# Kernel tuning notes

Hardware: AMD Instinct MI355X
Metric: run time of the kernel (lower is better)

## Reference

```python
import jax, jax.numpy as jnp
import numpy as np

C_IN = 512
C = 64        # per-head dim
N_HEAD = 8
B, S = 2, 2048


def setup_inputs() -> dict:
    key = jax.random.key(0)
    ks = jax.random.split(key, 9)
    scale = 1.0 / np.sqrt(C_IN)
    return {
        "x": jax.random.normal(ks[0], (B, S, C_IN), dtype=jnp.float32),
        "bias": jax.random.normal(ks[1], (B, N_HEAD, S, S), dtype=jnp.float32),
        "Wq": jax.random.normal(ks[2], (N_HEAD * C, C_IN), dtype=jnp.float32) * scale,
        "Wk": jax.random.normal(ks[3], (N_HEAD * C, C_IN), dtype=jnp.float32) * scale,
        "Wv": jax.random.normal(ks[4], (N_HEAD * C, C_IN), dtype=jnp.float32) * scale,
        "Wo": jax.random.normal(ks[5], (C_IN, N_HEAD * C), dtype=jnp.float32) * scale,
        "bo": jax.random.normal(ks[6], (C_IN,), dtype=jnp.float32) * 0.01,
        "Wg": jax.random.normal(ks[7], (N_HEAD * C, C_IN), dtype=jnp.float32) * scale,
        "bg": jax.random.normal(ks[8], (N_HEAD * C,), dtype=jnp.float32) * 0.01,
    }


def reference(x, bias, Wq, Wk, Wv, Wo, bo, Wg, bg):
    # x: [B, S, C_IN]; attn_dim=1 -> q/k/v axis is already at -2 after movedim.
    # Project and split heads: [B, S, H*C] -> [B, H, S, C]
    def split_heads(t):
        Bq, Sq, _ = t.shape
        return t.reshape(Bq, Sq, N_HEAD, C).transpose(0, 2, 1, 3)

    q = split_heads(x @ Wq.T) / jnp.sqrt(jnp.asarray(C, x.dtype))
    k = split_heads(x @ Wk.T)
    v = split_heads(x @ Wv.T)

    a = jnp.einsum("bhqc,bhkc->bhqk", q, k) + bias   # [B, H, S, S]
    a = jax.nn.softmax(a, axis=-1)
    o = jnp.einsum("bhqk,bhkc->bhqc", a, v)          # [B, H, S, C]

    # merge heads back: [B, S, H*C]
    o = o.transpose(0, 2, 1, 3).reshape(x.shape[0], x.shape[1], N_HEAD * C)
    g = jax.nn.sigmoid(x @ Wg.T + bg)
    o = g * o
    return o @ Wo.T + bo                              # [B, S, C_IN]
```

## Files before the change

kernel.cpp:

```cpp
#include <hip/hip_runtime.h>
#include <math.h>

#define BB 2
#define HH 8
#define SS 2048
#define CC 64
#define CIN 512
#define DDIM 512
#define MM (BB*SS)
#define KCHUNK 32
#define NCHUNK (SS / KCHUNK)
#define NBUF 4

#define LOG2E 1.4426950408889634f
#define SHIFT2 (16.0f * LOG2E)

using short8  = __attribute__((ext_vector_type(8))) short;
using float4v = __attribute__((ext_vector_type(4))) float;

__device__ __forceinline__ unsigned short tob(float f) {
    unsigned u = __float_as_uint(f);
    unsigned r = (u + 0x7fffu + ((u >> 16) & 1u)) >> 16;
    return (unsigned short)r;
}
__device__ __forceinline__ float fromb(unsigned short u) {
    return __uint_as_float(((unsigned)u) << 16);
}

#define GLDS(srcp, ldsp)                                                     \
    __builtin_amdgcn_global_load_lds(                                        \
        (const __attribute__((address_space(1))) void*)(srcp),               \
        (__attribute__((address_space(3))) void*)(ldsp), 16, 0, 0)

__global__ __launch_bounds__(256) void convert_all(
    const float* __restrict__ x,
    const float* __restrict__ wq, const float* __restrict__ wk,
    const float* __restrict__ wv, const float* __restrict__ wg,
    const float* __restrict__ wo,
    unsigned short* __restrict__ xb,
    unsigned short* __restrict__ wqb, unsigned short* __restrict__ wkb,
    unsigned short* __restrict__ wvb, unsigned short* __restrict__ wgb,
    unsigned short* __restrict__ wob)
{
    const int NX4 = MM * CIN / 4;
    int i = blockIdx.x * blockDim.x + threadIdx.x;
    const float* src; unsigned short* dst; float scale = 1.0f; int off;
    if (i < NX4) { src = x; dst = xb; off = i; }
    else {
        int j = i - NX4;
        int seg = j >> 16;
        off = j & 65535;
        if      (seg == 0) { src = wq; dst = wqb; scale = 0.125f * LOG2E; }
        else if (seg == 1) { src = wk; dst = wkb; }
        else if (seg == 2) { src = wv; dst = wvb; }
        else if (seg == 3) { src = wg; dst = wgb; }
        else               { src = wo; dst = wob; }
    }
    float4 v = ((const float4*)src)[off];
    ushort4 o;
    o.x = tob(v.x * scale); o.y = tob(v.y * scale);
    o.z = tob(v.z * scale); o.w = tob(v.w * scale);
    ((ushort4*)dst)[off] = o;
}

__global__ __launch_bounds__(256) void proj_gemm(
    const unsigned short* __restrict__ X,
    const unsigned short* __restrict__ Wq,
    const unsigned short* __restrict__ Wk,
    const unsigned short* __restrict__ Wv,
    const unsigned short* __restrict__ Wg,
    const float* __restrict__ bg,
    unsigned short* __restrict__ Qd,
    unsigned short* __restrict__ Kd,
    unsigned short* __restrict__ Vd,
    unsigned short* __restrict__ Gd)
{
    __shared__ __align__(16) unsigned short At[64][72];
    __shared__ __align__(16) unsigned short Bt[64][72];

    int mode = blockIdx.z;
    const unsigned short* W = (mode == 0) ? Wq : (mode == 1) ? Wk : (mode == 2) ? Wv : Wg;

    int m0 = blockIdx.y * 64;
    int n0 = blockIdx.x * 64;
    int tid = threadIdx.x;
    int w = tid >> 6, lane = tid & 63;
    int quad = lane >> 4, l16 = lane & 15;
    int wm = w & 1, wn = w >> 1;

    float4v acc[2][2];
    for (int a = 0; a < 2; ++a) for (int c = 0; c < 2; ++c) acc[a][c] = (float4v)0.0f;

    for (int kc = 0; kc < CIN; kc += 64) {
        for (int it = 0; it < 2; ++it) {
            int idx = it * 2048 + tid * 8;
            int row = idx >> 6, col = idx & 63;
            *(short8*)&At[row][col] = *(const short8*)&X[(size_t)(m0 + row) * CIN + kc + col];
            *(short8*)&Bt[row][col] = *(const short8*)&W[(size_t)(n0 + row) * CIN + kc + col];
        }
        __syncthreads();
        for (int ks = 0; ks < 2; ++ks) {
            short8 a0 = *(const short8*)&At[wm * 32 + l16][ks * 32 + quad * 8];
            short8 a1 = *(const short8*)&At[wm * 32 + 16 + l16][ks * 32 + quad * 8];
            short8 b0 = *(const short8*)&Bt[wn * 32 + l16][ks * 32 + quad * 8];
            short8 b1 = *(const short8*)&Bt[wn * 32 + 16 + l16][ks * 32 + quad * 8];
            acc[0][0] = __builtin_amdgcn_mfma_f32_16x16x32_bf16(a0, b0, acc[0][0], 0, 0, 0);
            acc[0][1] = __builtin_amdgcn_mfma_f32_16x16x32_bf16(a0, b1, acc[0][1], 0, 0, 0);
            acc[1][0] = __builtin_amdgcn_mfma_f32_16x16x32_bf16(a1, b0, acc[1][0], 0, 0, 0);
            acc[1][1] = __builtin_amdgcn_mfma_f32_16x16x32_bf16(a1, b1, acc[1][1], 0, 0, 0);
        }
        __syncthreads();
    }

    if (mode == 2) {
        for (int a = 0; a < 2; ++a) for (int c = 0; c < 2; ++c)
            for (int r = 0; r < 4; ++r) {
                int ml = wm * 32 + a * 16 + quad * 4 + r;
                int nl = wn * 32 + c * 16 + l16;
                At[nl][ml] = tob(acc[a][c][r]);
            }
        __syncthreads();
        int bi = m0 >> 11, h = n0 >> 6, s0 = m0 & 2047;
        int crow = tid >> 2, seg = tid & 3;
        unsigned short* dp = Vd + (((size_t)(bi * HH + h) * CC) + crow) * SS + s0 + seg * 16;
        *(short8*)dp       = *(const short8*)&At[crow][seg * 16];
        *(short8*)(dp + 8) = *(const short8*)&At[crow][seg * 16 + 8];
        return;
    }

    for (int a = 0; a < 2; ++a) for (int c = 0; c < 2; ++c)
        for (int r = 0; r < 4; ++r) {
            int gm = m0 + wm * 32 + a * 16 + quad * 4 + r;
            int gn = n0 + wn * 32 + c * 16 + l16;
            float v = acc[a][c][r];
            if (mode <= 1) {
                int bi = gm >> 11, s = gm & 2047, h = gn >> 6, cc = gn & 63;
                unsigned short* d = (mode == 0) ? Qd : Kd;
                d[(((size_t)(bi * HH + h) * SS) + s) * CC + cc] = tob(v);
            } else {
                float g = 1.0f / (1.0f + __expf(-(v + bg[gn])));
                Gd[(size_t)gm * DDIM + gn] = tob(g);
            }
        }
}

__global__ __launch_bounds__(256, 2) void attn_kernel(
    const unsigned short* __restrict__ Q,
    const unsigned short* __restrict__ K,
    const unsigned short* __restrict__ V,
    const float* __restrict__ bias,
    const unsigned short* __restrict__ G,
    unsigned short* __restrict__ Om)
{
    __shared__ __align__(16) unsigned short Kt[NBUF][32][64];
    __shared__ __align__(16) unsigned short Vt[NBUF][64][32];
    __shared__ __align__(16) float Bs[NBUF][64][32];
    __shared__ __align__(16) unsigned short Pt[4][16][40];

    int qb = blockIdx.x * 64;
    int bh = blockIdx.y;
    int b = bh >> 3, h = bh & 7;
    int tid = threadIdx.x;
    int w = tid >> 6, lane = tid & 63;
    int quad = lane >> 4, l16 = lane & 15;
    int swl = l16 & 7;
    int vsw = l16 & 3;

    int phase = (blockIdx.x + blockIdx.y) & (NCHUNK - 1);

    const unsigned short* Qbh = Q + (size_t)bh * SS * CC;
    const unsigned short* Kbh = K + (size_t)bh * SS * CC;
    const unsigned short* Vbh = V + (size_t)bh * CC * SS;
    const float* Bbh = bias + (size_t)bh * SS * SS;

    int qrow = qb + w * 16 + l16;
    short8 aq0 = *(const short8*)&Qbh[(size_t)qrow * CC + quad * 8];
    short8 aq1 = *(const short8*)&Qbh[(size_t)qrow * CC + 32 + quad * 8];

    float lsum[4] = {0.f, 0.f, 0.f, 0.f};
    float4v accO[4];
    for (int jn = 0; jn < 4; ++jn) accO[jn] = (float4v)0.0f;

    int row8 = lane >> 3;
    int kswz = (lane & 7) ^ row8;
    int row4 = lane >> 2;
    int vswz = (lane & 3) ^ (row4 & 3);

    auto STAGE = [&](int d, int kb) {
        GLDS(Kbh + (size_t)(kb + w * 8 + row8) * CC + kswz * 8, &Kt[d][w * 8][0]);
        GLDS(Vbh + (size_t)(w * 16 + row4) * SS + kb + vswz * 8, &Vt[d][w * 16][0]);
#pragma unroll
        for (int t = 0; t < 2; ++t)
            GLDS(Bbh + (size_t)(qb + w * 16 + t * 8 + row8) * SS + kb + (lane & 7) * 4,
                 &Bs[d][w * 16 + t * 8][0]);
    };

    STAGE(0, ((0 + phase) & (NCHUNK - 1)) * KCHUNK);
    STAGE(1, ((1 + phase) & (NCHUNK - 1)) * KCHUNK);
    STAGE(2, ((2 + phase) & (NCHUNK - 1)) * KCHUNK);

#pragma unroll 4
    for (int c = 0; c < NCHUNK; ++c) {
        int d = c & (NBUF - 1);
        __builtin_amdgcn_sched_barrier(0);
        if (c + 2 < NCHUNK) {
            asm volatile("s_waitcnt vmcnt(8)" ::: "memory");
        } else if (c + 1 < NCHUNK) {
            asm volatile("s_waitcnt vmcnt(4)" ::: "memory");
        } else {
            asm volatile("s_waitcnt vmcnt(0)" ::: "memory");
        }
        __builtin_amdgcn_sched_barrier(0);
        __builtin_amdgcn_s_barrier();
        __builtin_amdgcn_sched_barrier(0);

        if (c + 3 < NCHUNK)
            STAGE((c + 3) & (NBUF - 1), ((c + 3 + phase) & (NCHUNK - 1)) * KCHUNK);

        float4v sa[2];
#pragma unroll
        for (int j = 0; j < 2; ++j) sa[j] = (float4v)(-SHIFT2);
#pragma unroll
        for (int j = 0; j < 2; ++j) {
            short8 bk0 = *(const short8*)&Kt[d][j * 16 + l16][((quad    ) ^ swl) * 8];
            short8 bk1 = *(const short8*)&Kt[d][j * 16 + l16][((quad + 4) ^ swl) * 8];
            sa[j] = __builtin_amdgcn_mfma_f32_16x16x32_bf16(aq0, bk0, sa[j], 0, 0, 0);
            sa[j] = __builtin_amdgcn_mfma_f32_16x16x32_bf16(aq1, bk1, sa[j], 0, 0, 0);
        }

#pragma unroll
        for (int j = 0; j < 2; ++j)
#pragma unroll
            for (int r = 0; r < 4; ++r) {
                float bb = Bs[d][w * 16 + quad * 4 + r][j * 16 + l16];
                float p = __builtin_amdgcn_exp2f(fmaf(bb, LOG2E, sa[j][r]));
                lsum[r] += p;
                Pt[w][quad * 4 + r][j * 16 + l16] = tob(p);
            }

        {
            short8 ap = *(const short8*)&Pt[w][l16][quad * 8];
#pragma unroll
            for (int jn = 0; jn < 4; ++jn) {
                short8 bv = *(const short8*)&Vt[d][jn * 16 + l16][(quad ^ vsw) * 8];
                accO[jn] = __builtin_amdgcn_mfma_f32_16x16x32_bf16(ap, bv, accO[jn], 0, 0, 0);
            }
        }

        __builtin_amdgcn_sched_barrier(0);
        asm volatile("s_waitcnt lgkmcnt(0)" ::: "memory");
        __builtin_amdgcn_sched_barrier(0);
    }

    float rl[4];
#pragma unroll
    for (int r = 0; r < 4; ++r) {
        float s = lsum[r];
        s += __shfl_xor(s, 1, 64);
        s += __shfl_xor(s, 2, 64);
        s += __shfl_xor(s, 4, 64);
        s += __shfl_xor(s, 8, 64);
        rl[r] = 1.0f / s;
    }

    int mrow = b * SS + qb + w * 16 + quad * 4;
#pragma unroll
    for (int jn = 0; jn < 4; ++jn)
#pragma unroll
        for (int r = 0; r < 4; ++r) {
            int col = h * 64 + jn * 16 + l16;
            float g = fromb(G[(size_t)(mrow + r) * DDIM + col]);
            Om[(size_t)(mrow + r) * DDIM + col] = tob(accO[jn][r] * rl[r] * g);
        }
}

__global__ __launch_bounds__(256) void out_gemm(
    const unsigned short* __restrict__ Og,
    const unsigned short* __restrict__ W,
    const float* __restrict__ bo,
    float* __restrict__ out)
{
    __shared__ __align__(16) unsigned short At[64][72];
    __shared__ __align__(16) unsigned short Bt[64][72];

    int m0 = blockIdx.y * 64;
    int n0 = blockIdx.x * 64;
    int tid = threadIdx.x;
    int w = tid >> 6, lane = tid & 63;
    int quad = lane >> 4, l16 = lane & 15;
    int wm = w & 1, wn = w >> 1;

    float4v acc[2][2];
    for (int a = 0; a < 2; ++a) for (int c = 0; c < 2; ++c) acc[a][c] = (float4v)0.0f;

    for (int kc = 0; kc < DDIM; kc += 64) {
        for (int it = 0; it < 2; ++it) {
            int idx = it * 2048 + tid * 8;
            int row = idx >> 6, col = idx & 63;
            *(short8*)&At[row][col] = *(const short8*)&Og[(size_t)(m0 + row) * DDIM + kc + col];
            *(short8*)&Bt[row][col] = *(const short8*)&W[(size_t)(n0 + row) * DDIM + kc + col];
        }
        __syncthreads();
        for (int ks = 0; ks < 2; ++ks) {
            short8 a0 = *(const short8*)&At[wm * 32 + l16][ks * 32 + quad * 8];
            short8 a1 = *(const short8*)&At[wm * 32 + 16 + l16][ks * 32 + quad * 8];
            short8 b0 = *(const short8*)&Bt[wn * 32 + l16][ks * 32 + quad * 8];
            short8 b1 = *(const short8*)&Bt[wn * 32 + 16 + l16][ks * 32 + quad * 8];
            acc[0][0] = __builtin_amdgcn_mfma_f32_16x16x32_bf16(a0, b0, acc[0][0], 0, 0, 0);
            acc[0][1] = __builtin_amdgcn_mfma_f32_16x16x32_bf16(a0, b1, acc[0][1], 0, 0, 0);
            acc[1][0] = __builtin_amdgcn_mfma_f32_16x16x32_bf16(a1, b0, acc[1][0], 0, 0, 0);
            acc[1][1] = __builtin_amdgcn_mfma_f32_16x16x32_bf16(a1, b1, acc[1][1], 0, 0, 0);
        }
        __syncthreads();
    }

    for (int a = 0; a < 2; ++a) for (int c = 0; c < 2; ++c)
        for (int r = 0; r < 4; ++r) {
            int gm = m0 + wm * 32 + a * 16 + quad * 4 + r;
            int gn = n0 + wn * 32 + c * 16 + l16;
            out[(size_t)gm * DDIM + gn] = acc[a][c][r] + bo[gn];
        }
}

extern "C" void kernel_launch(void* const* d_in, const int* in_sizes, int n_in,
                              void* d_out, int out_size, void* d_ws, size_t ws_size,
                              hipStream_t stream)
{
    const float* x    = (const float*)d_in[0];
    const float* bias = (const float*)d_in[1];
    const float* Wq   = (const float*)d_in[2];
    const float* Wk   = (const float*)d_in[3];
    const float* Wv   = (const float*)d_in[4];
    const float* Wo   = (const float*)d_in[5];
    const float* bo   = (const float*)d_in[6];
    const float* Wg   = (const float*)d_in[7];
    const float* bg   = (const float*)d_in[8];
    float* out = (float*)d_out;

    char* ws = (char*)d_ws;
    auto alloc = [&](size_t bytes) { char* p = ws; ws += (bytes + 255) & ~(size_t)255; return p; };
    unsigned short* xb  = (unsigned short*)alloc((size_t)MM * CIN * 2);
    unsigned short* wqb = (unsigned short*)alloc((size_t)DDIM * CIN * 2);
    unsigned short* wkb = (unsigned short*)alloc((size_t)DDIM * CIN * 2);
    unsigned short* wvb = (unsigned short*)alloc((size_t)DDIM * CIN * 2);
    unsigned short* wgb = (unsigned short*)alloc((size_t)DDIM * CIN * 2);
    unsigned short* wob = (unsigned short*)alloc((size_t)DDIM * CIN * 2);
    unsigned short* Qh  = (unsigned short*)alloc((size_t)BB * HH * SS * CC * 2);
    unsigned short* Kh  = (unsigned short*)alloc((size_t)BB * HH * SS * CC * 2);
    unsigned short* Vh  = (unsigned short*)alloc((size_t)BB * HH * SS * CC * 2);
    unsigned short* Gt  = (unsigned short*)alloc((size_t)MM * DDIM * 2);
    unsigned short* Om  = (unsigned short*)alloc((size_t)MM * DDIM * 2);

    convert_all<<<3328, 256, 0, stream>>>(x, Wq, Wk, Wv, Wg, Wo,
                                          xb, wqb, wkb, wvb, wgb, wob);
    proj_gemm<<<dim3(DDIM / 64, MM / 64, 4), 256, 0, stream>>>(
        xb, wqb, wkb, wvb, wgb, bg, Qh, Kh, Vh, Gt);
    attn_kernel<<<dim3(SS / 64, BB * HH), 256, 0, stream>>>(
        Qh, Kh, Vh, bias, Gt, Om);
    out_gemm<<<dim3(DDIM / 64, MM / 64), 256, 0, stream>>>(Om, wob, bo, out);
}
```

Measured before the change: 463.9 us.

## Replace LDS-staged K/V/bias pipeline with direct global loads and register double-buffered bias

The attention kernel no longer stages K, V and bias tiles through a multi-buffered LDS ring with global_load_lds and block barriers. Each wave now reads K and V fragments straight from global memory into MFMA operands and prefetches its bias values into registers one chunk ahead. The key chunk grows from 32 to 64, and LDS now holds only the P tile. This removes block-wide barriers and LDS traffic, at the cost of redundant global/L2 reads of K and V across the four waves, higher register pressure, and bias loads that are only 4-byte scalar accesses.

```diff
diff --git a/kernel.cpp b/kernel.cpp
--- a/kernel.cpp
+++ b/kernel.cpp
@@ -8,9 +8,8 @@
 #define CIN 512
 #define DDIM 512
 #define MM (BB*SS)
-#define KCHUNK 32
+#define KCHUNK 64
 #define NCHUNK (SS / KCHUNK)
-#define NBUF 4
 
 #define LOG2E 1.4426950408889634f
 #define SHIFT2 (16.0f * LOG2E)
@@ -26,11 +25,6 @@
 __device__ __forceinline__ float fromb(unsigned short u) {
     return __uint_as_float(((unsigned)u) << 16);
 }
-
-#define GLDS(srcp, ldsp)                                                     \
-    __builtin_amdgcn_global_load_lds(                                        \
-        (const __attribute__((address_space(1))) void*)(srcp),               \
-        (__attribute__((address_space(3))) void*)(ldsp), 16, 0, 0)
 
 __global__ __launch_bounds__(256) void convert_all(
     const float* __restrict__ x,
@@ -152,10 +146,7 @@
     const unsigned short* __restrict__ G,
     unsigned short* __restrict__ Om)
 {
-    __shared__ __align__(16) unsigned short Kt[NBUF][32][64];
-    __shared__ __align__(16) unsigned short Vt[NBUF][64][32];
-    __shared__ __align__(16) float Bs[NBUF][64][32];
-    __shared__ __align__(16) unsigned short Pt[4][16][40];
+    __shared__ __align__(16) unsigned short Pt[4][16][72];
 
     int qb = blockIdx.x * 64;
     int bh = blockIdx.y;
@@ -163,15 +154,14 @@
     int tid = threadIdx.x;
     int w = tid >> 6, lane = tid & 63;
     int quad = lane >> 4, l16 = lane & 15;
-    int swl = l16 & 7;
-    int vsw = l16 & 3;
 
     int phase = (blockIdx.x + blockIdx.y) & (NCHUNK - 1);
 
     const unsigned short* Qbh = Q + (size_t)bh * SS * CC;
     const unsigned short* Kbh = K + (size_t)bh * SS * CC;
     const unsigned short* Vbh = V + (size_t)bh * CC * SS;
-    const float* Bbh = bias + (size_t)bh * SS * SS;
+    const float* brow = bias + (size_t)bh * SS * SS
+                      + (size_t)(qb + w * 16 + quad * 4) * SS + l16;
 
     int qrow = qb + w * 16 + l16;
     short8 aq0 = *(const short8*)&Qbh[(size_t)qrow * CC + quad * 8];
@@ -181,75 +171,83 @@
     float4v accO[4];
     for (int jn = 0; jn < 4; ++jn) accO[jn] = (float4v)0.0f;
 
-    int row8 = lane >> 3;
-    int kswz = (lane & 7) ^ row8;
-    int row4 = lane >> 2;
-    int vswz = (lane & 3) ^ (row4 & 3);
-
-    auto STAGE = [&](int d, int kb) {
-        GLDS(Kbh + (size_t)(kb + w * 8 + row8) * CC + kswz * 8, &Kt[d][w * 8][0]);
-        GLDS(Vbh + (size_t)(w * 16 + row4) * SS + kb + vswz * 8, &Vt[d][w * 16][0]);
-#pragma unroll
-        for (int t = 0; t < 2; ++t)
-            GLDS(Bbh + (size_t)(qb + w * 16 + t * 8 + row8) * SS + kb + (lane & 7) * 4,
-                 &Bs[d][w * 16 + t * 8][0]);
-    };
-
-    STAGE(0, ((0 + phase) & (NCHUNK - 1)) * KCHUNK);
-    STAGE(1, ((1 + phase) & (NCHUNK - 1)) * KCHUNK);
-    STAGE(2, ((2 + phase) & (NCHUNK - 1)) * KCHUNK);
-
-#pragma unroll 4
-    for (int c = 0; c < NCHUNK; ++c) {
-        int d = c & (NBUF - 1);
-        __builtin_amdgcn_sched_barrier(0);
+#define DECLB(S) float S##00,S##01,S##02,S##03, S##10,S##11,S##12,S##13, \
+                       S##20,S##21,S##22,S##23, S##30,S##31,S##32,S##33
+#define LDB(S, kb) do {                                                   \
+    S##00 = brow[0*SS+(kb)   ]; S##01 = brow[1*SS+(kb)   ];               \
+    S##02 = brow[2*SS+(kb)   ]; S##03 = brow[3*SS+(kb)   ];               \
+    S##10 = brow[0*SS+(kb)+16]; S##11 = brow[1*SS+(kb)+16];               \
+    S##12 = brow[2*SS+(kb)+16]; S##13 = brow[3*SS+(kb)+16];               \
+    S##20 = brow[0*SS+(kb)+32]; S##21 = brow[1*SS+(kb)+32];               \
+    S##22 = brow[2*SS+(kb)+32]; S##23 = brow[3*SS+(kb)+32];               \
+    S##30 = brow[0*SS+(kb)+48]; S##31 = brow[1*SS+(kb)+48];               \
+    S##32 = brow[2*SS+(kb)+48]; S##33 = brow[3*SS+(kb)+48];               \
+} while (0)
+
+#define PEXP(saj, B0, B1, B2, B3, jj) do {                                 \
+    float p0 = __builtin_amdgcn_exp2f(fmaf(B0, LOG2E, (saj)[0]));          \
+    float p1 = __builtin_amdgcn_exp2f(fmaf(B1, LOG2E, (saj)[1]));          \
+    float p2 = __builtin_amdgcn_exp2f(fmaf(B2, LOG2E, (saj)[2]));          \
+    float p3 = __builtin_amdgcn_exp2f(fmaf(B3, LOG2E, (saj)[3]));          \
+    lsum[0] += p0; lsum[1] += p1; lsum[2] += p2; lsum[3] += p3;            \
+    Pt[w][quad * 4 + 0][(jj) * 16 + l16] = tob(p0);                        \
+    Pt[w][quad * 4 + 1][(jj) * 16 + l16] = tob(p1);                        \
+    Pt[w][quad * 4 + 2][(jj) * 16 + l16] = tob(p2);                        \
+    Pt[w][quad * 4 + 3][(jj) * 16 + l16] = tob(p3);                        \
+} while (0)
+
+#define BODY(S, kb) do {                                                   \
+    float4v sa0 = (float4v)(-SHIFT2), sa1 = (float4v)(-SHIFT2);            \
+    float4v sa2 = (float4v)(-SHIFT2), sa3 = (float4v)(-SHIFT2);            \
+    {                                                                      \
+        short8 k0, k1;                                                     \
+        k0 = *(const short8*)&Kbh[(size_t)((kb) +  0 + l16) * CC + quad * 8];      \
+        k1 = *(const short8*)&Kbh[(size_t)((kb) +  0 + l16) * CC + 32 + quad * 8]; \
+        sa0 = __builtin_amdgcn_mfma_f32_16x16x32_bf16(aq0, k0, sa0, 0, 0, 0);      \
+        sa0 = __builtin_amdgcn_mfma_f32_16x16x32_bf16(aq1, k1, sa0, 0, 0, 0);      \
+        k0 = *(const short8*)&Kbh[(size_t)((kb) + 16 + l16) * CC + quad * 8];      \
+        k1 = *(const short8*)&Kbh[(size_t)((kb) + 16 + l16) * CC + 32 + quad * 8]; \
+        sa1 = __builtin_amdgcn_mfma_f32_16x16x32_bf16(aq0, k0, sa1, 0, 0, 0);      \
+        sa1 = __builtin_amdgcn_mfma_f32_16x16x32_bf16(aq1, k1, sa1, 0, 0, 0);      \
+        k0 = *(const short8*)&Kbh[(size_t)((kb) + 32 + l16) * CC + quad * 8];      \
+        k1 = *(const short8*)&Kbh[(size_t)((kb) + 32 + l16) * CC + 32 + quad * 8]; \
+        sa2 = __builtin_amdgcn_mfma_f32_16x16x32_bf16(aq0, k0, sa2, 0, 0, 0);      \
+        sa2 = __builtin_amdgcn_mfma_f32_16x16x32_bf16(aq1, k1, sa2, 0, 0, 0);      \
+        k0 = *(const short8*)&Kbh[(size_t)((kb) + 48 + l16) * CC + quad * 8];      \
+        k1 = *(const short8*)&Kbh[(size_t)((kb) + 48 + l16) * CC + 32 + quad * 8]; \
+        sa3 = __builtin_amdgcn_mfma_f32_16x16x32_bf16(aq0, k0, sa3, 0, 0, 0);      \
+        sa3 = __builtin_amdgcn_mfma_f32_16x16x32_bf16(aq1, k1, sa3, 0, 0, 0);      \
+    }                                                                      \
+    PEXP(sa0, S##00, S##01, S##02, S##03, 0);                              \
+    PEXP(sa1, S##10, S##11, S##12, S##13, 1);                              \
+    PEXP(sa2, S##20, S##21, S##22, S##23, 2);                              \
+    PEXP(sa3, S##30, S##31, S##32, S##33, 3);                              \
+    _Pragma("unroll")                                                      \
+    for (int ks = 0; ks < 2; ++ks) {                                       \
+        short8 ap = *(const short8*)&Pt[w][l16][ks * 32 + quad * 8];       \
+        _Pragma("unroll")                                                  \
+        for (int jn = 0; jn < 4; ++jn) {                                   \
+            short8 bv = *(const short8*)&Vbh[(size_t)(jn * 16 + l16) * SS  \
+                                             + (kb) + ks * 32 + quad * 8]; \
+            accO[jn] = __builtin_amdgcn_mfma_f32_16x16x32_bf16(ap, bv, accO[jn], 0, 0, 0); \
+        }                                                                  \
+    }                                                                      \
+} while (0)
+
+    DECLB(bA); DECLB(bB);
+
+    LDB(bA, (phase & (NCHUNK - 1)) * KCHUNK);
+
+    for (int c = 0; c < NCHUNK; c += 2) {
+        int ka = ((c     + phase) & (NCHUNK - 1)) * KCHUNK;
+        int kb_ = ((c + 1 + phase) & (NCHUNK - 1)) * KCHUNK;
+        LDB(bB, kb_);
+        BODY(bA, ka);
         if (c + 2 < NCHUNK) {
-            asm volatile("s_waitcnt vmcnt(8)" ::: "memory");
-        } else if (c + 1 < NCHUNK) {
-            asm volatile("s_waitcnt vmcnt(4)" ::: "memory");
-        } else {
-            asm volatile("s_waitcnt vmcnt(0)" ::: "memory");
-        }
-        __builtin_amdgcn_sched_barrier(0);
-        __builtin_amdgcn_s_barrier();
-        __builtin_amdgcn_sched_barrier(0);
-
-        if (c + 3 < NCHUNK)
-            STAGE((c + 3) & (NBUF - 1), ((c + 3 + phase) & (NCHUNK - 1)) * KCHUNK);
-
-        float4v sa[2];
-#pragma unroll
-        for (int j = 0; j < 2; ++j) sa[j] = (float4v)(-SHIFT2);
-#pragma unroll
-        for (int j = 0; j < 2; ++j) {
-            short8 bk0 = *(const short8*)&Kt[d][j * 16 + l16][((quad    ) ^ swl) * 8];
-            short8 bk1 = *(const short8*)&Kt[d][j * 16 + l16][((quad + 4) ^ swl) * 8];
-            sa[j] = __builtin_amdgcn_mfma_f32_16x16x32_bf16(aq0, bk0, sa[j], 0, 0, 0);
-            sa[j] = __builtin_amdgcn_mfma_f32_16x16x32_bf16(aq1, bk1, sa[j], 0, 0, 0);
-        }
-
-#pragma unroll
-        for (int j = 0; j < 2; ++j)
-#pragma unroll
-            for (int r = 0; r < 4; ++r) {
-                float bb = Bs[d][w * 16 + quad * 4 + r][j * 16 + l16];
-                float p = __builtin_amdgcn_exp2f(fmaf(bb, LOG2E, sa[j][r]));
-                lsum[r] += p;
-                Pt[w][quad * 4 + r][j * 16 + l16] = tob(p);
-            }
-
-        {
-            short8 ap = *(const short8*)&Pt[w][l16][quad * 8];
-#pragma unroll
-            for (int jn = 0; jn < 4; ++jn) {
-                short8 bv = *(const short8*)&Vt[d][jn * 16 + l16][(quad ^ vsw) * 8];
-                accO[jn] = __builtin_amdgcn_mfma_f32_16x16x32_bf16(ap, bv, accO[jn], 0, 0, 0);
-            }
-        }
-
-        __builtin_amdgcn_sched_barrier(0);
-        asm volatile("s_waitcnt lgkmcnt(0)" ::: "memory");
-        __builtin_amdgcn_sched_barrier(0);
+            int kn = ((c + 2 + phase) & (NCHUNK - 1)) * KCHUNK;
+            LDB(bA, kn);
+        }
+        BODY(bB, kb_);
     }
 
     float rl[4];
@@ -272,6 +270,10 @@
             float g = fromb(G[(size_t)(mrow + r) * DDIM + col]);
             Om[(size_t)(mrow + r) * DDIM + col] = tob(accO[jn][r] * rl[r] * g);
         }
+#undef DECLB
+#undef LDB
+#undef PEXP
+#undef BODY
 }
 
 __global__ __launch_bounds__(256) void out_gemm(
```

Measured after the change: 498.7 us. 7.5% more time.
